# Kernel optimization log

Hardware: AMD Instinct MI355X
Metric: run time of the kernel (lower is better)

The kernel has to match this reference:

```python
import jax, jax.numpy as jnp
import numpy as np

HIDDEN = 1024
HEADS = 16
HEAD_DIM = HIDDEN // HEADS
NEG_INF = -1.0e9


def setup_inputs() -> dict:
    key = jax.random.key(0)
    ks = jax.random.split(key, 9)
    B, S = 4, 2048
    scale = 1.0 / np.sqrt(HIDDEN)
    inp = {
        'query': jax.random.normal(ks[0], (B, S, HIDDEN), dtype=jnp.float32),
        'masks': jnp.ones((B, S), dtype=jnp.float32),
        'Wq': jax.random.normal(ks[1], (HIDDEN, HIDDEN), dtype=jnp.float32) * scale,
        'bq': jnp.zeros((HIDDEN,), dtype=jnp.float32),
        'Wk': jax.random.normal(ks[2], (HIDDEN, HIDDEN), dtype=jnp.float32) * scale,
        'bk': jnp.zeros((HIDDEN,), dtype=jnp.float32),
        'Wv': jax.random.normal(ks[3], (HIDDEN, HIDDEN), dtype=jnp.float32) * scale,
        'bv': jnp.zeros((HIDDEN,), dtype=jnp.float32),
        'Wo': jax.random.normal(ks[4], (HIDDEN, HIDDEN), dtype=jnp.float32) * scale,
        'bo': jnp.zeros((HIDDEN,), dtype=jnp.float32),
    }
    return inp


def _split_heads(x):
    # [B, S, H*D] -> [B, H, S, D]
    B, S, C = x.shape
    return x.reshape(B, S, HEADS, C // HEADS).transpose(0, 2, 1, 3)


def reference(query, masks, Wq, bq, Wk, bk, Wv, bv, Wo, bo):
    # torch Linear: y = x @ W.T + b
    q = query @ Wq.T + bq
    k = query @ Wk.T + bk
    v = query @ Wv.T + bv
    qh = _split_heads(q) * (HEAD_DIM ** -0.5)  # [B,H,S,D]
    kh = _split_heads(k)
    vh = _split_heads(v)
    bias = ((1.0 - masks) * NEG_INF)[:, None, None, :]  # [B,1,1,S]
    logits = jnp.einsum('bhqd,bhkd->bhqk', qh, kh) + bias
    weights = jax.nn.softmax(logits, axis=-1)  # dropout p=0.0 -> identity
    x = jnp.einsum('bhqk,bhkd->bhqd', weights, vh)  # [B,H,S,D]
    B, H, S, D = x.shape
    combined = x.transpose(0, 2, 1, 3).reshape(B, S, H * D)
    return combined @ Wo.T + bo
```

## Files before the change

kernel.cpp:

```cpp
#include <hip/hip_runtime.h>

typedef unsigned short u16;
typedef unsigned int u32;
typedef u16 u16x4 __attribute__((ext_vector_type(4)));
typedef u16 u16x8 __attribute__((ext_vector_type(8)));
typedef u32 u32x4 __attribute__((ext_vector_type(4)));
typedef __bf16 bf16x8 __attribute__((ext_vector_type(8)));
typedef float f32x4 __attribute__((ext_vector_type(4)));

#define GPTR(p) (const __attribute__((address_space(1))) void*)(p)
#define LPTR(p) (__attribute__((address_space(3))) void*)(p)
#define ASYNC16(g, l) __builtin_amdgcn_global_load_lds(GPTR(g), LPTR(l), 16, 0, 0)

#if __has_builtin(__builtin_amdgcn_exp2f)
#define EXP2(x) __builtin_amdgcn_exp2f(x)
#else
#define EXP2(x) __builtin_exp2f(x)
#endif

__device__ __forceinline__ u16 f2bf(float f) {
    u32 u = __builtin_bit_cast(u32, f);
    return (u16)((u + 0x7fffu + ((u >> 16) & 1u)) >> 16);
}
__device__ __forceinline__ bf16x8 ld8(const void* p) {
    return __builtin_bit_cast(bf16x8, *(const u16x8*)p);
}

__global__ void cvt_f32_bf16(const float* __restrict__ in, u16* __restrict__ out, int n4) {
    int i = blockIdx.x * blockDim.x + threadIdx.x;
    if (i >= n4) return;
    float4 v = ((const float4*)in)[i];
    ushort4 o;
    o.x = f2bf(v.x); o.y = f2bf(v.y); o.z = f2bf(v.z); o.w = f2bf(v.w);
    ((ushort4*)out)[i] = o;
}

template<int MODE>
__global__ __launch_bounds__(256, 2) void gemm_bt(
    const u16* __restrict__ A, const u16* __restrict__ B,
    const float* __restrict__ b0, const float* __restrict__ b1, const float* __restrict__ b2,
    u16* __restrict__ O0, u16* __restrict__ O1, u16* __restrict__ O2,
    float* __restrict__ OF)
{
    constexpr int K = 1024;
    __shared__ __align__(16) u16 As[128 * 32];
    __shared__ __align__(16) u16 Bs[128 * 32];
    const int tid = threadIdx.x;
    const int wave = tid >> 6, lane = tid & 63;
    const int m0 = blockIdx.y * 128, n0 = blockIdx.x * 128;
    const int wm = (wave >> 1) * 64, wn = (wave & 1) * 64;
    const int fr = lane & 15, fg = lane >> 4;

    f32x4 acc[4][4] = {};

    const int srow = lane >> 2;
    const int scol = (lane & 3) * 8;
    const u16* aSrc = A + (size_t)(m0 + wave * 32 + srow) * K + scol;
    const u16* bSrc = B + (size_t)(n0 + wave * 32 + srow) * K + scol;
    u16* const aDst0 = &As[(wave * 32) * 32];
    u16* const aDst1 = &As[(wave * 32 + 16) * 32];
    u16* const bDst0 = &Bs[(wave * 32) * 32];
    u16* const bDst1 = &Bs[(wave * 32 + 16) * 32];

    for (int kt = 0; kt < K; kt += 32) {
        ASYNC16(aSrc + kt,          aDst0);
        ASYNC16(aSrc + kt + 16 * K, aDst1);
        ASYNC16(bSrc + kt,          bDst0);
        ASYNC16(bSrc + kt + 16 * K, bDst1);
        __syncthreads();
        bf16x8 af[4], bfv[4];
        #pragma unroll
        for (int i = 0; i < 4; ++i) af[i]  = ld8(&As[(wm + i * 16 + fr) * 32 + fg * 8]);
        #pragma unroll
        for (int j = 0; j < 4; ++j) bfv[j] = ld8(&Bs[(wn + j * 16 + fr) * 32 + fg * 8]);
        #pragma unroll
        for (int i = 0; i < 4; ++i)
            #pragma unroll
            for (int j = 0; j < 4; ++j)
                acc[i][j] = __builtin_amdgcn_mfma_f32_16x16x32_bf16(af[i], bfv[j], acc[i][j], 0, 0, 0);
        __syncthreads();
    }

    if constexpr (MODE == 0) {
        const float QSCALE = 0.125f * 1.44269504f;
        #pragma unroll
        for (int j = 0; j < 4; ++j) {
            const int n = n0 + wn + j * 16 + fr;
            const int sel = n >> 10;
            const int w = n & 1023;
            const float bb = (sel == 0 ? b0 : sel == 1 ? b1 : b2)[w];
            const int h = w >> 6, d = w & 63;
            if (sel == 2) {
                #pragma unroll
                for (int i = 0; i < 4; ++i) {
                    const int m = m0 + wm + i * 16 + fg * 4;
                    u16x4 st;
                    #pragma unroll
                    for (int r = 0; r < 4; ++r) st[r] = f2bf(acc[i][j][r] + bb);
                    *(u16x4*)&O2[((size_t)(((m >> 11) * 16 + h) * 64 + d)) * 2048 + (m & 2047)] = st;
                }
            } else {
                const float scale = (sel == 0) ? QSCALE : 1.0f;
                u16* const dst = (sel == 0 ? O0 : O1);
                #pragma unroll
                for (int i = 0; i < 4; ++i) {
                    #pragma unroll
                    for (int r = 0; r < 4; ++r) {
                        const int m = m0 + wm + i * 16 + fg * 4 + r;
                        dst[(((size_t)((m >> 11) * 16 + h) * 2048 + (m & 2047)) << 6) + d] =
                            f2bf((acc[i][j][r] + bb) * scale);
                    }
                }
            }
        }
    } else {
        #pragma unroll
        for (int j = 0; j < 4; ++j) {
            const int n = n0 + wn + j * 16 + fr;
            const float bb = b0[n];
            #pragma unroll
            for (int i = 0; i < 4; ++i) {
                #pragma unroll
                for (int r = 0; r < 4; ++r) {
                    const int m = m0 + wm + i * 16 + fg * 4 + r;
                    OF[(size_t)m * 1024 + n] = acc[i][j][r] + bb;
                }
            }
        }
    }
}

__global__ __launch_bounds__(256, 4) void attn_fwd(
    const u16* __restrict__ Qg, const u16* __restrict__ Kg, const u16* __restrict__ Vt,
    const float* __restrict__ masks, u16* __restrict__ X2)
{
    __shared__ __align__(16) char smem[32768];
    const int tid = threadIdx.x;
    const int wave = tid >> 6, lane = tid & 63;

    const int bidL = blockIdx.x;
    const int wg = ((bidL & 7) << 7) | (bidL >> 3);
    const int bh = wg >> 4;
    const int q0 = (wg & 15) * 128 + wave * 32;
    const int b = bh >> 4, h = bh & 15;
    const int fr = lane & 15, fg = lane >> 4;
    const int swz = (fr & 7) << 4;

    const int a0 = fr * 128 + ((fg * 16) ^ swz);
    const int a1 = fr * 128 + ((64 + fg * 16) ^ swz);

    bf16x8 qf[2][2];
    #pragma unroll
    for (int qs = 0; qs < 2; ++qs) {
        const u16* qp = Qg + ((size_t)bh * 2048 + q0 + qs * 16 + fr) * 64 + fg * 8;
        qf[qs][0] = ld8(qp);
        qf[qs][1] = ld8(qp + 32);
    }

    f32x4 o[4][2] = {};
    f32x4 den[2] = {};
    const f32x4 FZ = {0.f, 0.f, 0.f, 0.f};
    const u16x8 ONE_BITS = {0x3F80,0x3F80,0x3F80,0x3F80,0x3F80,0x3F80,0x3F80,0x3F80};
    const bf16x8 ONES = __builtin_bit_cast(bf16x8, ONE_BITS);

    const int srow = lane >> 3;
    const int scb = (lane & 7) * 16;
    const float* mrow = masks + b * 2048;

    auto STAGE = [&](int buf, int kv0) {
        #pragma unroll
        for (int j = 0; j < 2; ++j) {
            const int r0 = wave * 16 + j * 8;
            const int row = r0 + srow;
            const int sw = scb ^ ((row & 7) << 4);
            ASYNC16((const char*)(Kg + ((size_t)bh * 2048 + kv0 + row) * 64) + sw,
                    smem + buf * 8192 + r0 * 128);
            ASYNC16((const char*)(Vt + ((size_t)bh * 64 + row) * 2048 + kv0) + sw,
                    smem + 16384 + buf * 8192 + r0 * 128);
        }
    };

    const int t0 = (((bidL >> 8) & 3) << 3);
    STAGE(0, t0 * 64);
    for (int it = 0; it < 32; it += 2) {
        #pragma unroll
        for (int half = 0; half < 2; ++half) {
            const int tile = (t0 + it + half) & 31;
            const int kv = tile * 64;
            const int kb = half * 8192;
            const int vb = 16384 + half * 8192;
            __syncthreads();
            if (it + half < 31) STAGE(half ^ 1, ((tile + 1) & 31) * 64);

            float4 mv[4];
            #pragma unroll
            for (int nj = 0; nj < 4; ++nj)
                mv[nj] = *(const float4*)(mrow + kv + nj * 16 + fg * 4);

            #pragma unroll
            for (int hh = 0; hh < 2; ++hh) {
                const int aK = hh ? a1 : a0;
                f32x4 s[2][2];
                #pragma unroll
                for (int njl = 0; njl < 2; ++njl) {
                    const int nj = hh * 2 + njl;
                    bf16x8 k0 = ld8(smem + kb + nj * 2048 + a0);
                    bf16x8 k1 = ld8(smem + kb + nj * 2048 + a1);
                    __builtin_amdgcn_s_setprio(1);
                    #pragma unroll
                    for (int qs = 0; qs < 2; ++qs) {
                        f32x4 z = __builtin_amdgcn_mfma_f32_16x16x32_bf16(k0, qf[qs][0], FZ, 0, 0, 0);
                        s[njl][qs] = __builtin_amdgcn_mfma_f32_16x16x32_bf16(k1, qf[qs][1], z, 0, 0, 0);
                    }
                    __builtin_amdgcn_s_setprio(0);
                }
                #pragma unroll
                for (int njl = 0; njl < 2; ++njl) {
                    const int nj = hh * 2 + njl;
                    #pragma unroll
                    for (int qs = 0; qs < 2; ++qs)
                        #pragma unroll
                        for (int r = 0; r < 4; ++r)
                            s[njl][qs][r] = EXP2(s[njl][qs][r]) * mv[nj][r];
                }
                bf16x8 pa[2];
                #pragma unroll
                for (int qs = 0; qs < 2; ++qs) {
                    u32 m0, m1, m2, m3;
                    asm("v_cvt_pk_bf16_f32 %0, %1, %2" : "=v"(m0) : "v"(s[0][qs][0]), "v"(s[0][qs][1]));
                    asm("v_cvt_pk_bf16_f32 %0, %1, %2" : "=v"(m1) : "v"(s[0][qs][2]), "v"(s[0][qs][3]));
                    asm("v_cvt_pk_bf16_f32 %0, %1, %2" : "=v"(m2) : "v"(s[1][qs][0]), "v"(s[1][qs][1]));
                    asm("v_cvt_pk_bf16_f32 %0, %1, %2" : "=v"(m3) : "v"(s[1][qs][2]), "v"(s[1][qs][3]));
                    asm("v_permlane32_swap_b32 %0, %1" : "+v"(m0), "+v"(m2));
                    asm("v_permlane32_swap_b32 %0, %1" : "+v"(m1), "+v"(m3));
                    asm("v_permlane16_swap_b32 %0, %1" : "+v"(m0), "+v"(m2));
                    asm("v_permlane16_swap_b32 %0, %1" : "+v"(m1), "+v"(m3));
                    pa[qs] = __builtin_bit_cast(bf16x8, u32x4{m0, m1, m2, m3});
                }

                __builtin_amdgcn_s_setprio(1);
                #pragma unroll
                for (int qs = 0; qs < 2; ++qs)
                    den[qs] = __builtin_amdgcn_mfma_f32_16x16x32_bf16(ONES, pa[qs], den[qs], 0, 0, 0);
                #pragma unroll
                for (int dj = 0; dj < 4; ++dj) {
                    bf16x8 v = ld8(smem + vb + dj * 2048 + aK);
                    #pragma unroll
                    for (int qs = 0; qs < 2; ++qs)
                        o[dj][qs] = __builtin_amdgcn_mfma_f32_16x16x32_bf16(v, pa[qs], o[dj][qs], 0, 0, 0);
                }
                __builtin_amdgcn_s_setprio(0);
            }
        }
    }

    #pragma unroll
    for (int qs = 0; qs < 2; ++qs) {
        const float inv = 1.0f / den[qs][0];
        const int q = q0 + qs * 16 + fr;
        u16* dst = X2 + ((size_t)(b * 2048 + q)) * 1024 + h * 64 + fg * 4;
        #pragma unroll
        for (int dj = 0; dj < 4; ++dj) {
            u16x4 st;
            #pragma unroll
            for (int r = 0; r < 4; ++r) st[r] = f2bf(o[dj][qs][r] * inv);
            *(u16x4*)(dst + dj * 16) = st;
        }
    }
}

extern "C" void kernel_launch(void* const* d_in, const int* in_sizes, int n_in,
                              void* d_out, int out_size, void* d_ws, size_t ws_size,
                              hipStream_t stream) {
    const float* query = (const float*)d_in[0];
    const float* masks = (const float*)d_in[1];
    const float* Wq = (const float*)d_in[2];
    const float* bq = (const float*)d_in[3];
    const float* Wk = (const float*)d_in[4];
    const float* bk = (const float*)d_in[5];
    const float* Wv = (const float*)d_in[6];
    const float* bv = (const float*)d_in[7];
    const float* Wo = (const float*)d_in[8];
    const float* bo = (const float*)d_in[9];
    float* out = (float*)d_out;

    char* ws = (char*)d_ws;
    u16* Xb   = (u16*)(ws);
    u16* Wcat = (u16*)(ws + (16u << 20));
    u16* Wob  = (u16*)(ws + (22u << 20));
    u16* Qg   = (u16*)(ws + (24u << 20));
    u16* Kg   = (u16*)(ws + (40u << 20));
    u16* Vt   = (u16*)(ws + (56u << 20));
    u16* X2   = Xb;

    cvt_f32_bf16<<<8192, 256, 0, stream>>>(query, Xb, 8192 * 1024 / 4);
    cvt_f32_bf16<<<1024, 256, 0, stream>>>(Wq, Wcat,               1024 * 1024 / 4);
    cvt_f32_bf16<<<1024, 256, 0, stream>>>(Wk, Wcat + 1024 * 1024, 1024 * 1024 / 4);
    cvt_f32_bf16<<<1024, 256, 0, stream>>>(Wv, Wcat + 2 * 1024 * 1024, 1024 * 1024 / 4);
    cvt_f32_bf16<<<1024, 256, 0, stream>>>(Wo, Wob, 1024 * 1024 / 4);

    gemm_bt<0><<<dim3(24, 64), 256, 0, stream>>>(Xb, Wcat, bq, bk, bv, Qg, Kg, Vt, nullptr);
    attn_fwd<<<1024, 256, 0, stream>>>(Qg, Kg, Vt, masks, X2);
    gemm_bt<1><<<dim3(8, 64), 256, 0, stream>>>(X2, Wob, bo, nullptr, nullptr, nullptr,
                                                nullptr, nullptr, out);
}
```

Before: 196.6 us.

## Fuse conversion launches and skip mask multiply when mask row is all ones

Merges the five f32-to-bf16 conversion launches into a single kernel that selects its source and destination by block index, removing launch overhead. In attention, each block first scans its batch's mask row and, if every entry is exactly 1, runs a templated KV loop that skips the per-tile mask loads and multiplies. The general masked path is kept, so results stay correct for arbitrary masks, at the cost of an extra 8 KB mask read per block and a duplicated loop body.

```diff
diff --git a/kernel.cpp b/kernel.cpp
--- a/kernel.cpp
+++ b/kernel.cpp
@@ -26,13 +26,29 @@
     return __builtin_bit_cast(bf16x8, *(const u16x8*)p);
 }
 
-__global__ void cvt_f32_bf16(const float* __restrict__ in, u16* __restrict__ out, int n4) {
-    int i = blockIdx.x * blockDim.x + threadIdx.x;
-    if (i >= n4) return;
-    float4 v = ((const float4*)in)[i];
-    ushort4 o;
-    o.x = f2bf(v.x); o.y = f2bf(v.y); o.z = f2bf(v.z); o.w = f2bf(v.w);
-    ((ushort4*)out)[i] = o;
+__global__ void cvt_all(const float* __restrict__ q,
+                        const float* __restrict__ wq, const float* __restrict__ wk,
+                        const float* __restrict__ wv, const float* __restrict__ wo,
+                        u16* __restrict__ xb, u16* __restrict__ wcat, u16* __restrict__ wob) {
+    const int blk = blockIdx.x;
+    const float* src;
+    u16* dst;
+    size_t base;
+    if (blk < 8192) {
+        src = q; dst = xb; base = (size_t)blk * 256;
+    } else {
+        const int t = blk - 8192;
+        const int w = t >> 10;
+        base = (size_t)(t & 1023) * 256;
+        src = (w == 0) ? wq : (w == 1) ? wk : (w == 2) ? wv : wo;
+        dst = (w == 0) ? wcat : (w == 1) ? wcat + 1024 * 1024
+            : (w == 2) ? wcat + 2 * 1024 * 1024 : wob;
+    }
+    const size_t i = base + threadIdx.x;
+    float4 v = ((const float4*)src)[i];
+    ushort4 o4;
+    o4.x = f2bf(v.x); o4.y = f2bf(v.y); o4.z = f2bf(v.z); o4.w = f2bf(v.w);
+    ((ushort4*)dst)[i] = o4;
 }
 
 template<int MODE>
@@ -130,57 +146,26 @@
     }
 }
 
-__global__ __launch_bounds__(256, 4) void attn_fwd(
-    const u16* __restrict__ Qg, const u16* __restrict__ Kg, const u16* __restrict__ Vt,
-    const float* __restrict__ masks, u16* __restrict__ X2)
+template<bool MASKED>
+__device__ __forceinline__ void kv_loop(
+    char* smem, const u16* __restrict__ Kbh, const u16* __restrict__ Vtbh,
+    const float* __restrict__ mrow, int wave, int fg, int a0, int a1, int t0,
+    int srow, int scb, bf16x8 (&qf)[2][2], f32x4 (&o)[4][2], f32x4 (&den)[2],
+    const f32x4& FZ, const bf16x8& ONES)
 {
-    __shared__ __align__(16) char smem[32768];
-    const int tid = threadIdx.x;
-    const int wave = tid >> 6, lane = tid & 63;
-
-    const int bidL = blockIdx.x;
-    const int wg = ((bidL & 7) << 7) | (bidL >> 3);
-    const int bh = wg >> 4;
-    const int q0 = (wg & 15) * 128 + wave * 32;
-    const int b = bh >> 4, h = bh & 15;
-    const int fr = lane & 15, fg = lane >> 4;
-    const int swz = (fr & 7) << 4;
-
-    const int a0 = fr * 128 + ((fg * 16) ^ swz);
-    const int a1 = fr * 128 + ((64 + fg * 16) ^ swz);
-
-    bf16x8 qf[2][2];
-    #pragma unroll
-    for (int qs = 0; qs < 2; ++qs) {
-        const u16* qp = Qg + ((size_t)bh * 2048 + q0 + qs * 16 + fr) * 64 + fg * 8;
-        qf[qs][0] = ld8(qp);
-        qf[qs][1] = ld8(qp + 32);
-    }
-
-    f32x4 o[4][2] = {};
-    f32x4 den[2] = {};
-    const f32x4 FZ = {0.f, 0.f, 0.f, 0.f};
-    const u16x8 ONE_BITS = {0x3F80,0x3F80,0x3F80,0x3F80,0x3F80,0x3F80,0x3F80,0x3F80};
-    const bf16x8 ONES = __builtin_bit_cast(bf16x8, ONE_BITS);
-
-    const int srow = lane >> 3;
-    const int scb = (lane & 7) * 16;
-    const float* mrow = masks + b * 2048;
-
     auto STAGE = [&](int buf, int kv0) {
         #pragma unroll
         for (int j = 0; j < 2; ++j) {
             const int r0 = wave * 16 + j * 8;
             const int row = r0 + srow;
             const int sw = scb ^ ((row & 7) << 4);
-            ASYNC16((const char*)(Kg + ((size_t)bh * 2048 + kv0 + row) * 64) + sw,
+            ASYNC16((const char*)(Kbh + (size_t)(kv0 + row) * 64) + sw,
                     smem + buf * 8192 + r0 * 128);
-            ASYNC16((const char*)(Vt + ((size_t)bh * 64 + row) * 2048 + kv0) + sw,
+            ASYNC16((const char*)(Vtbh + (size_t)row * 2048 + kv0) + sw,
                     smem + 16384 + buf * 8192 + r0 * 128);
         }
     };
 
-    const int t0 = (((bidL >> 8) & 3) << 3);
     STAGE(0, t0 * 64);
     for (int it = 0; it < 32; it += 2) {
         #pragma unroll
@@ -193,9 +178,11 @@
             if (it + half < 31) STAGE(half ^ 1, ((tile + 1) & 31) * 64);
 
             float4 mv[4];
-            #pragma unroll
-            for (int nj = 0; nj < 4; ++nj)
-                mv[nj] = *(const float4*)(mrow + kv + nj * 16 + fg * 4);
+            if (MASKED) {
+                #pragma unroll
+                for (int nj = 0; nj < 4; ++nj)
+                    mv[nj] = *(const float4*)(mrow + kv + nj * 16 + fg * 4);
+            }
 
             #pragma unroll
             for (int hh = 0; hh < 2; ++hh) {
@@ -220,8 +207,11 @@
                     #pragma unroll
                     for (int qs = 0; qs < 2; ++qs)
                         #pragma unroll
-                        for (int r = 0; r < 4; ++r)
-                            s[njl][qs][r] = EXP2(s[njl][qs][r]) * mv[nj][r];
+                        for (int r = 0; r < 4; ++r) {
+                            float p = EXP2(s[njl][qs][r]);
+                            if (MASKED) p *= mv[nj][r];
+                            s[njl][qs][r] = p;
+                        }
                 }
                 bf16x8 pa[2];
                 #pragma unroll
@@ -253,6 +243,67 @@
             }
         }
     }
+}
+
+__global__ __launch_bounds__(256, 4) void attn_fwd(
+    const u16* __restrict__ Qg, const u16* __restrict__ Kg, const u16* __restrict__ Vt,
+    const float* __restrict__ masks, u16* __restrict__ X2)
+{
+    __shared__ __align__(16) char smem[32768];
+    const int tid = threadIdx.x;
+    const int wave = tid >> 6, lane = tid & 63;
+
+    const int bidL = blockIdx.x;
+    const int wg = ((bidL & 7) << 7) | (bidL >> 3);
+    const int bh = wg >> 4;
+    const int q0 = (wg & 15) * 128 + wave * 32;
+    const int b = bh >> 4, h = bh & 15;
+    const int fr = lane & 15, fg = lane >> 4;
+    const int swz = (fr & 7) << 4;
+
+    const int a0 = fr * 128 + ((fg * 16) ^ swz);
+    const int a1 = fr * 128 + ((64 + fg * 16) ^ swz);
+
+    const u16* const Kbh  = Kg + (size_t)bh * 2048 * 64;
+    const u16* const Vtbh = Vt + (size_t)bh * 64 * 2048;
+    const float* mrow = masks + b * 2048;
+
+    bf16x8 qf[2][2];
+    #pragma unroll
+    for (int qs = 0; qs < 2; ++qs) {
+        const u16* qp = Qg + ((size_t)bh * 2048 + q0 + qs * 16 + fr) * 64 + fg * 8;
+        qf[qs][0] = ld8(qp);
+        qf[qs][1] = ld8(qp + 32);
+    }
+
+    bool ok = true;
+    {
+        const float4* mp = (const float4*)mrow;
+        #pragma unroll
+        for (int i = 0; i < 8; ++i) {
+            float4 m = mp[lane + i * 64];
+            ok = ok && (m.x == 1.0f) && (m.y == 1.0f) && (m.z == 1.0f) && (m.w == 1.0f);
+        }
+        ok = __all(ok);
+    }
+
+    f32x4 o[4][2] = {};
+    f32x4 den[2] = {};
+    const f32x4 FZ = {0.f, 0.f, 0.f, 0.f};
+    const u16x8 ONE_BITS = {0x3F80,0x3F80,0x3F80,0x3F80,0x3F80,0x3F80,0x3F80,0x3F80};
+    const bf16x8 ONES = __builtin_bit_cast(bf16x8, ONE_BITS);
+
+    const int srow = lane >> 3;
+    const int scb = (lane & 7) * 16;
+
+    const int t0 = (((bidL >> 8) & 3) << 3);
+
+    if (ok)
+        kv_loop<false>(smem, Kbh, Vtbh, mrow, wave, fg, a0, a1, t0, srow, scb,
+                       qf, o, den, FZ, ONES);
+    else
+        kv_loop<true>(smem, Kbh, Vtbh, mrow, wave, fg, a0, a1, t0, srow, scb,
+                      qf, o, den, FZ, ONES);
 
     #pragma unroll
     for (int qs = 0; qs < 2; ++qs) {
@@ -293,12 +344,7 @@
     u16* Vt   = (u16*)(ws + (56u << 20));
     u16* X2   = Xb;
 
-    cvt_f32_bf16<<<8192, 256, 0, stream>>>(query, Xb, 8192 * 1024 / 4);
-    cvt_f32_bf16<<<1024, 256, 0, stream>>>(Wq, Wcat,               1024 * 1024 / 4);
-    cvt_f32_bf16<<<1024, 256, 0, stream>>>(Wk, Wcat + 1024 * 1024, 1024 * 1024 / 4);
-    cvt_f32_bf16<<<1024, 256, 0, stream>>>(Wv, Wcat + 2 * 1024 * 1024, 1024 * 1024 / 4);
-    cvt_f32_bf16<<<1024, 256, 0, stream>>>(Wo, Wob, 1024 * 1024 / 4);
-
+    cvt_all<<<12288, 256, 0, stream>>>(query, Wq, Wk, Wv, Wo, Xb, Wcat, Wob);
     gemm_bt<0><<<dim3(24, 64), 256, 0, stream>>>(Xb, Wcat, bq, bk, bv, Qg, Kg, Vt, nullptr);
     attn_fwd<<<1024, 256, 0, stream>>>(Qg, Kg, Vt, masks, X2);
     gemm_bt<1><<<dim3(8, 64), 256, 0, stream>>>(X2, Wob, bo, nullptr, nullptr, nullptr,
```

Result: faster. 186.6 us (-5.1%).
